# Optimization experiments

Hardware: AMD Instinct MI355X
Metric: run time of the kernel (lower is better)

The kernel has to match this reference:

```python
import jax, jax.numpy as jnp
import numpy as np

N = 50000       # nodes
E = 800000      # directed edges (src -> dst)
INDIM, HID, OUT = 256, 128, 64
NEG_SLOPE = 0.2  # PyG GATConv default negative_slope


def gat_layer(x, src, dst, W, a_src, a_dst, b, n_nodes):
    """Single-head PyG-style GATConv with self-loops already in (src, dst)."""
    h = x @ W.T                                   # [N, F_out]
    alpha_src = h @ a_src                         # [N]
    alpha_dst = h @ a_dst                         # [N]
    # per-edge attention logits, LeakyReLU
    e = jax.nn.leaky_relu(alpha_src[src] + alpha_dst[dst], NEG_SLOPE)  # [E']
    # segment softmax grouped by destination node (numerically stable)
    m = jnp.full((n_nodes,), -jnp.inf, e.dtype).at[dst].max(e)
    ee = jnp.exp(e - m[dst])
    denom = jax.ops.segment_sum(ee, dst, num_segments=n_nodes)
    alpha = ee / denom[dst]                       # [E']
    # weighted scatter-add of source messages
    out = jax.ops.segment_sum(h[src] * alpha[:, None], dst, num_segments=n_nodes)
    return out + b


def setup_inputs() -> dict:
    key = jax.random.key(0)
    ks = jax.random.split(key, 10)
    s = 0.1
    return {
        "x": jax.random.normal(ks[0], (N, INDIM), jnp.float32),
        "edge_index": jax.random.randint(ks[1], (2, E), 0, N, dtype=jnp.int32),
        "W1": jax.random.normal(ks[2], (HID, INDIM), jnp.float32) * s,
        "a_src1": jax.random.normal(ks[3], (HID,), jnp.float32) * s,
        "a_dst1": jax.random.normal(ks[4], (HID,), jnp.float32) * s,
        "b1": jnp.zeros((HID,), jnp.float32),
        "W2": jax.random.normal(ks[5], (OUT, HID), jnp.float32) * s,
        "a_src2": jax.random.normal(ks[6], (OUT,), jnp.float32) * s,
        "a_dst2": jax.random.normal(ks[7], (OUT,), jnp.float32) * s,
        "b2": jnp.zeros((OUT,), jnp.float32),
    }


def reference(x, edge_index, W1, a_src1, a_dst1, b1, W2, a_src2, a_dst2, b2):
    n_nodes = x.shape[0]
    # PyG GATConv default add_self_loops=True
    loops = jnp.arange(n_nodes, dtype=edge_index.dtype)
    src = jnp.concatenate([edge_index[0], loops])
    dst = jnp.concatenate([edge_index[1], loops])
    h = gat_layer(x, src, dst, W1, a_src1, a_dst1, b1, n_nodes)
    h = jax.nn.relu(h)
    h = gat_layer(h, src, dst, W2, a_src2, a_dst2, b2, n_nodes)
    return h
```

## Files before the change

### kernel.cpp

```cpp
#include <hip/hip_runtime.h>
#include <hip/hip_bf16.h>
#include <math.h>

#define NN 50000
#define EE 800000
#define INDIM 256
#define HID 128
#define OUTF 64
#define NEG_SLOPE 0.2f
#define CAP 64

#define NB ((NN + 255) >> 8)
#define BCAP 6144
#define CHUNK 2048
#define EPT 8
#define BPAD 16

typedef __attribute__((ext_vector_type(8))) short bf16x8;
typedef __attribute__((ext_vector_type(4))) float f32x4;

__device__ inline float bflo(unsigned p) { return __uint_as_float(p << 16); }
__device__ inline float bfhi(unsigned p) { return __uint_as_float(p & 0xffff0000u); }
__device__ inline unsigned f2bf(float f) {
    unsigned u = __float_as_uint(f);
    return (u + 0x7fffu + ((u >> 16) & 1u)) >> 16;
}
__device__ inline unsigned cvt_pk_bf16(float lo, float hi) {
    unsigned r;
    asm("v_cvt_pk_bf16_f32 %0, %1, %2" : "=v"(r) : "v"(lo), "v"(hi));
    return r;
}
__device__ inline float leaky(float l) { return (l > 0.f) ? l : NEG_SLOPE * l; }

template <typename AT, int BM, int BN, int WR, int WC, bool FA, bool FAL>
__device__ inline void gemm_body(const AT* __restrict__ A,
                                 const float* __restrict__ B,
                                 unsigned short* __restrict__ Cb,
                                 const float* __restrict__ a_s,
                                 const float* __restrict__ a_d,
                                 float* __restrict__ asrc,
                                 float* __restrict__ adst,
                                 int N, int K, int bid)
{
    constexpr int LD = 40;
    constexpr int MF = (BM / WR) / 16;
    constexpr int NF = (BN / WC) / 16;
    constexpr int NA  = (sizeof(AT) == 4) ? (BM * 8 / 256) : (BM * 4 / 256);
    constexpr int NBL = BN * 8 / 256;
    static_assert(!FA || WC == 1, "register alpha needs full cols per wave");
    __shared__ unsigned short As[BM * LD];
    __shared__ unsigned short Bs[BN * LD];
    __shared__ float al_s[FAL ? 2 * BM : 2];

    const int tid = threadIdx.x;
    const int wave = tid >> 6, lane = tid & 63;
    const int wr = wave / WC, wc = wave % WC;
    const int wrow0 = wr * (BM / WR);
    const int wcol0 = wc * (BN / WC);
    const int row0 = bid * BM;
    const int lrow = lane & 15, lkg = lane >> 4;

    if constexpr (FAL) {
        for (int i = tid; i < 2 * BM; i += 256) al_s[i] = 0.f;
    }

    int arow[NA], aoff[NA]; bool aval[NA];
    #pragma unroll
    for (int u = 0; u < NA; ++u) {
        int i = u * 256 + tid;
        if constexpr (sizeof(AT) == 4) { arow[u] = i >> 3; aoff[u] = (i & 7) * 4; }
        else                           { arow[u] = i >> 2; aoff[u] = (i & 3) * 8; }
        aval[u] = (row0 + arow[u]) < N;
    }
    int brow[NBL], boff[NBL];
    #pragma unroll
    for (int u = 0; u < NBL; ++u) {
        int i = u * 256 + tid;
        brow[u] = i >> 3; boff[u] = (i & 7) * 4;
    }

    uint4 ra[NA], rb[NBL];
    auto loadA = [&](int k0) {
        #pragma unroll
        for (int u = 0; u < NA; ++u) {
            ra[u] = make_uint4(0u, 0u, 0u, 0u);
            if (aval[u])
                ra[u] = *(const uint4*)((const AT*)A + (size_t)(row0 + arow[u]) * K + k0 + aoff[u]);
        }
    };
    auto loadB = [&](int k0) {
        #pragma unroll
        for (int u = 0; u < NBL; ++u)
            rb[u] = *(const uint4*)(B + (size_t)brow[u] * K + k0 + boff[u]);
    };
    auto storeLDS = [&]() {
        if constexpr (sizeof(AT) == 4) {
            #pragma unroll
            for (int u = 0; u < NA; ++u) {
                unsigned p0 = cvt_pk_bf16(__uint_as_float(ra[u].x), __uint_as_float(ra[u].y));
                unsigned p1 = cvt_pk_bf16(__uint_as_float(ra[u].z), __uint_as_float(ra[u].w));
                *(uint2*)&As[arow[u] * LD + aoff[u]] = make_uint2(p0, p1);
            }
        } else {
            #pragma unroll
            for (int u = 0; u < NA; ++u)
                *(uint4*)&As[arow[u] * LD + aoff[u]] = ra[u];
        }
        #pragma unroll
        for (int u = 0; u < NBL; ++u) {
            unsigned p0 = cvt_pk_bf16(__uint_as_float(rb[u].x), __uint_as_float(rb[u].y));
            unsigned p1 = cvt_pk_bf16(__uint_as_float(rb[u].z), __uint_as_float(rb[u].w));
            *(uint2*)&Bs[brow[u] * LD + boff[u]] = make_uint2(p0, p1);
        }
    };

    f32x4 acc[MF][NF];
    #pragma unroll
    for (int mi = 0; mi < MF; ++mi)
        #pragma unroll
        for (int ni = 0; ni < NF; ++ni) acc[mi][ni] = 0.f;

    const int NK = K / 32;
    loadA(0); loadB(0);
    for (int ks = 0; ks < NK; ++ks) {
        storeLDS();
        __syncthreads();
        if (ks + 1 < NK) { loadA((ks + 1) * 32); loadB((ks + 1) * 32); }

        bf16x8 af[MF], bfr[NF];
        #pragma unroll
        for (int mi = 0; mi < MF; ++mi)
            af[mi] = *(const bf16x8*)&As[(wrow0 + mi * 16 + lrow) * LD + lkg * 8];
        #pragma unroll
        for (int ni = 0; ni < NF; ++ni)
            bfr[ni] = *(const bf16x8*)&Bs[(wcol0 + ni * 16 + lrow) * LD + lkg * 8];
        #pragma unroll
        for (int mi = 0; mi < MF; ++mi)
            #pragma unroll
            for (int ni = 0; ni < NF; ++ni)
                acc[mi][ni] = __builtin_amdgcn_mfma_f32_16x16x32_bf16(
                    af[mi], bfr[ni], acc[mi][ni], 0, 0, 0);
        __syncthreads();
    }

    if constexpr (FA || FAL) {
        float asv[NF], adv[NF];
        #pragma unroll
        for (int ni = 0; ni < NF; ++ni) {
            int c = wcol0 + ni * 16 + lrow;
            asv[ni] = a_s[c]; adv[ni] = a_d[c];
        }
        #pragma unroll
        for (int mi = 0; mi < MF; ++mi)
            #pragma unroll
            for (int r = 0; r < 4; ++r) {
                float ps = 0.f, pd = 0.f;
                #pragma unroll
                for (int ni = 0; ni < NF; ++ni) {
                    ps = fmaf(acc[mi][ni][r], asv[ni], ps);
                    pd = fmaf(acc[mi][ni][r], adv[ni], pd);
                }
                #pragma unroll
                for (int d = 1; d < 16; d <<= 1) {
                    ps += __shfl_xor(ps, d);
                    pd += __shfl_xor(pd, d);
                }
                int lr_ = wrow0 + mi * 16 + lkg * 4 + r;
                if constexpr (FA) {
                    int gr = row0 + lr_;
                    if (lrow == 0 && gr < N) { asrc[gr] = ps; adst[gr] = pd; }
                } else {
                    if (lrow == 0) {
                        atomicAdd(&al_s[lr_], ps);
                        atomicAdd(&al_s[BM + lr_], pd);
                    }
                }
            }
    }

    #pragma unroll
    for (int mi = 0; mi < MF; ++mi)
        #pragma unroll
        for (int ni = 0; ni < NF; ++ni)
            #pragma unroll
            for (int r = 0; r < 4; ++r) {
                int gr = row0 + wrow0 + mi * 16 + lkg * 4 + r;
                int gc = wcol0 + ni * 16 + lrow;
                if (gr < N)
                    Cb[(size_t)gr * BN + gc] = (unsigned short)f2bf(acc[mi][ni][r]);
            }

    if constexpr (FAL) {
        __syncthreads();
        if (tid < BM) {
            int gr = row0 + tid;
            if (gr < N) { asrc[gr] = al_s[tid]; adst[gr] = al_s[BM + tid]; }
        }
    }
}

__global__ __launch_bounds__(256) void gemm1_kernel(
    const float* __restrict__ x, const float* __restrict__ W1,
    unsigned short* __restrict__ h1b,
    const float* __restrict__ a_s, const float* __restrict__ a_d,
    float* __restrict__ asrc, float* __restrict__ adst, int N, int K)
{
    gemm_body<float, 64, 128, 2, 2, false, true>(x, W1, h1b, a_s, a_d,
                                                 asrc, adst, N, K, blockIdx.x);
}

__global__ __launch_bounds__(256) void gemm2_alpha_kernel(
    const unsigned short* __restrict__ A, const float* __restrict__ B,
    unsigned short* __restrict__ Cb,
    const float* __restrict__ a_s, const float* __restrict__ a_d,
    float* __restrict__ asrc, float* __restrict__ adst, int N, int K)
{
    gemm_body<unsigned short, 64, 64, 4, 1, true, false>(A, B, Cb, a_s, a_d,
                                                         asrc, adst, N, K, blockIdx.x);
}

__global__ __launch_bounds__(256) void bin_kernel(
    const int* __restrict__ src_in, const int* __restrict__ dst_in,
    unsigned* __restrict__ gbucket, int* __restrict__ bcnt,
    int E, int tot)
{
    __shared__ int h_hist[256];
    __shared__ int h_scan[256];
    __shared__ int h_ofs[256];
    __shared__ int h_gbase[256];
    __shared__ unsigned grp[CHUNK];

    const int tid = threadIdx.x;
    const int e0 = blockIdx.x * CHUNK;
    const int cntc = min(CHUNK, tot - e0);

    h_hist[tid] = 0;
    __syncthreads();

    unsigned pk[EPT];
    bool val[EPT];
    #pragma unroll
    for (int u = 0; u < EPT; ++u) {
        int e = e0 + u * 256 + tid;
        val[u] = (e < tot);
        if (val[u]) {
            int d, s;
            if (e < E) { d = dst_in[e]; s = src_in[e]; }
            else       { d = e - E;    s = d; }
            pk[u] = ((unsigned)d << 16) | (unsigned)s;
            atomicAdd(&h_hist[d >> 8], 1);
        }
    }
    __syncthreads();

    int v = h_hist[tid];
    int incl = v;
    h_scan[tid] = incl;
    __syncthreads();
    for (int off = 1; off < 256; off <<= 1) {
        int t = (tid >= off) ? h_scan[tid - off] : 0;
        __syncthreads();
        incl += t;
        h_scan[tid] = incl;
        __syncthreads();
    }
    int excl = incl - v;
    h_scan[tid] = excl;
    h_ofs[tid] = excl;
    h_gbase[tid] = (tid < NB && v > 0) ? atomicAdd(&bcnt[tid * BPAD], v) : 0;
    __syncthreads();

    #pragma unroll
    for (int u = 0; u < EPT; ++u)
        if (val[u]) {
            int b = pk[u] >> 24;
            int pos = atomicAdd(&h_ofs[b], 1);
            grp[pos] = pk[u];
        }
    __syncthreads();

    for (int i = tid; i < cntc; i += 256) {
        unsigned p = grp[i];
        int b = p >> 24;
        int gp = h_gbase[b] + (i - h_scan[b]);
        if (gp < BCAP) gbucket[(size_t)b * BCAP + gp] = p;
    }
}

__global__ __launch_bounds__(256) void csr_build(
    const unsigned* __restrict__ gbucket, const int* __restrict__ bcnt,
    int* __restrict__ cnt, unsigned short* __restrict__ csr, int N)
{
    __shared__ int c2[256];
    __shared__ unsigned short cl[256 * CAP];

    const int b = blockIdx.x;
    const int tid = threadIdx.x;
    c2[tid] = 0;
    __syncthreads();

    int len = bcnt[b * BPAD];
    if (len > BCAP) len = BCAP;
    for (int i = tid; i < len; i += 256) {
        unsigned p = gbucket[(size_t)b * BCAP + i];
        int dl = (p >> 16) & 255;
        int s  = p & 0xffff;
        int r = atomicAdd(&c2[dl], 1);
        if (r < CAP) cl[(dl << 6) + r] = (unsigned short)s;
    }
    __syncthreads();

    int d = (b << 8) + tid;
    if (d < N) cnt[d] = c2[tid];

    int rows = N - (b << 8);
    rows = (rows > 256) ? 256 : rows;
    const uint4* sp = (const uint4*)cl;
    uint4* dp = (uint4*)(csr + (((size_t)b << 8) << 6));
    for (int i = tid; i < rows * 8; i += 256) dp[i] = sp[i];
}

template <int F, bool RELU, bool OUTBF>
__global__ __launch_bounds__(256) void aggregate_kernel(
    const unsigned short* __restrict__ hb, const unsigned short* __restrict__ csr,
    const int* __restrict__ cnt_arr, const float* __restrict__ asrc,
    const float* __restrict__ adst, const float* __restrict__ bias,
    void* __restrict__ outv, int n)
{
    constexpr int G = F / 8;
    constexpr int EPI = 64 / G;
    constexpr int STEP = EPI * 4;
    int wave = (int)((blockIdx.x * (size_t)blockDim.x + threadIdx.x) >> 6);
    int lane = threadIdx.x & 63;
    if (wave >= n) return;
    const size_t beg = (size_t)wave << 6;
    int cntv = cnt_arr[wave];
    cntv = (cntv > CAP) ? CAP : cntv;
    const float ad = adst[wave];
    const int grp = lane / G, fl = lane % G;

    float acc[8];
    #pragma unroll
    for (int p = 0; p < 8; ++p) acc[p] = 0.f;

    int s = 0;
    float e = 0.f;
    if (lane < cntv) { s = (int)csr[beg + lane]; e = __expf(leaky(asrc[s] + ad)); }
    float denom = e;
    #pragma unroll
    for (int d = 32; d > 0; d >>= 1) denom += __shfl_xor(denom, d);
    float w = e * __fdividef(1.f, denom);

    for (int jj0 = 0; jj0 < cntv; jj0 += STEP) {
        uint4 q[4];
        float wj[4];
        #pragma unroll
        for (int u = 0; u < 4; ++u) {
            int sel = jj0 + u * EPI + grp;
            int sj = __shfl(s, sel);
            wj[u] = __shfl(w, sel);
            q[u] = make_uint4(0u, 0u, 0u, 0u);
            if (sel < cntv)
                q[u] = *(const uint4*)(hb + (size_t)sj * F + fl * 8);
        }
        #pragma unroll
        for (int u = 0; u < 4; ++u) {
            acc[0] += wj[u] * bflo(q[u].x); acc[1] += wj[u] * bfhi(q[u].x);
            acc[2] += wj[u] * bflo(q[u].y); acc[3] += wj[u] * bfhi(q[u].y);
            acc[4] += wj[u] * bflo(q[u].z); acc[5] += wj[u] * bfhi(q[u].z);
            acc[6] += wj[u] * bflo(q[u].w); acc[7] += wj[u] * bfhi(q[u].w);
        }
    }

    #pragma unroll
    for (int d = G; d < 64; d <<= 1)
        #pragma unroll
        for (int p = 0; p < 8; ++p) acc[p] += __shfl_xor(acc[p], d);

    if (lane < G) {
        float v[8];
        #pragma unroll
        for (int p = 0; p < 8; ++p) {
            v[p] = acc[p] + bias[fl * 8 + p];
            if (RELU) v[p] = fmaxf(v[p], 0.f);
        }
        if constexpr (OUTBF) {
            unsigned short* o = (unsigned short*)outv + (size_t)wave * F + fl * 8;
            uint4 pk;
            pk.x = cvt_pk_bf16(v[0], v[1]);
            pk.y = cvt_pk_bf16(v[2], v[3]);
            pk.z = cvt_pk_bf16(v[4], v[5]);
            pk.w = cvt_pk_bf16(v[6], v[7]);
            *(uint4*)o = pk;
        } else {
            float* o = (float*)outv + (size_t)wave * F + fl * 8;
            *(float4*)o       = make_float4(v[0], v[1], v[2], v[3]);
            *(float4*)(o + 4) = make_float4(v[4], v[5], v[6], v[7]);
        }
    }
}

extern "C" void kernel_launch(void* const* d_in, const int* in_sizes, int n_in,
                              void* d_out, int out_size, void* d_ws, size_t ws_size,
                              hipStream_t stream)
{
    const float* x      = (const float*)d_in[0];
    const int*   ei     = (const int*)d_in[1];
    const float* W1     = (const float*)d_in[2];
    const float* a_src1 = (const float*)d_in[3];
    const float* a_dst1 = (const float*)d_in[4];
    const float* b1     = (const float*)d_in[5];
    const float* W2     = (const float*)d_in[6];
    const float* a_src2 = (const float*)d_in[7];
    const float* a_dst2 = (const float*)d_in[8];
    const float* b2     = (const float*)d_in[9];
    float* out = (float*)d_out;

    const int N = NN, E = EE;
    const int* src_in = ei;
    const int* dst_in = ei + E;

    char* p = (char*)d_ws;
    unsigned short* h1b   = (unsigned short*)p; p += (size_t)N * HID * 2;
    unsigned short* hmidb = (unsigned short*)p; p += (size_t)N * HID * 2;
    unsigned short* h2b   = (unsigned short*)p; p += (size_t)N * OUTF * 2;
    float* asrc = (float*)p; p += (size_t)N * 4;
    float* adst = (float*)p; p += (size_t)N * 4;
    int* cnt    = (int*)p;   p += (size_t)N * 4;
    unsigned short* csr = (unsigned short*)p; p += (size_t)N * CAP * 2;
    int* bcnt = (int*)p; p += (size_t)NB * BPAD * 4;
    unsigned* gbucket = (unsigned*)h2b;

    hipMemsetAsync(bcnt, 0, (size_t)NB * BPAD * 4, stream);

    const int GB   = (N + 63) / 64;
    const int BINB = (E + N + CHUNK - 1) / CHUNK;
    const int nwb  = (N * 64 + 255) / 256;

    bin_kernel<<<BINB, 256, 0, stream>>>(src_in, dst_in, gbucket, bcnt, E, E + N);
    csr_build<<<NB, 256, 0, stream>>>(gbucket, bcnt, cnt, csr, N);

    gemm1_kernel<<<GB, 256, 0, stream>>>(x, W1, h1b, a_src1, a_dst1,
                                         asrc, adst, N, INDIM);
    aggregate_kernel<HID, true, true><<<nwb, 256, 0, stream>>>(
        h1b, csr, cnt, asrc, adst, b1, hmidb, N);

    gemm2_alpha_kernel<<<GB, 256, 0, stream>>>(hmidb, W2, h2b, a_src2, a_dst2,
                                               asrc, adst, N, HID);
    aggregate_kernel<OUTF, false, false><<<nwb, 256, 0, stream>>>(
        h2b, csr, cnt, asrc, adst, b2, out, N);

    (void)in_sizes; (void)n_in; (void)out_size; (void)ws_size;
}
```

Baseline: 206.2 us.

## Fuse gemm1 with edge binning and layer-1 aggregation with gemm2

The layer-1 GEMM and the edge binning kernel now run as one launch, with block-index ranges dispatching to either body so the two independent jobs share the GPU. The layer-1 aggregation is fused with the layer-2 GEMM: each 256-thread block aggregates 64 nodes into a bf16 tile in shared memory, then runs MFMA against W2 and computes the layer-2 attention scalars. This removes the hidden-feature round trip through global memory and two launches. In exchange, the aggregation runs with far fewer blocks, each wave handling 16 nodes in sequence, which may reduce latency hiding for the gathers.

```diff
diff --git a/kernel.cpp b/kernel.cpp
--- a/kernel.cpp
+++ b/kernel.cpp
@@ -32,7 +32,7 @@
 }
 __device__ inline float leaky(float l) { return (l > 0.f) ? l : NEG_SLOPE * l; }
 
-template <typename AT, int BM, int BN, int WR, int WC, bool FA, bool FAL>
+template <typename AT, int BM, int BN, int WR, int WC, bool FAL>
 __device__ inline void gemm_body(const AT* __restrict__ A,
                                  const float* __restrict__ B,
                                  unsigned short* __restrict__ Cb,
@@ -47,7 +47,6 @@
     constexpr int NF = (BN / WC) / 16;
     constexpr int NA  = (sizeof(AT) == 4) ? (BM * 8 / 256) : (BM * 4 / 256);
     constexpr int NBL = BN * 8 / 256;
-    static_assert(!FA || WC == 1, "register alpha needs full cols per wave");
     __shared__ unsigned short As[BM * LD];
     __shared__ unsigned short Bs[BN * LD];
     __shared__ float al_s[FAL ? 2 * BM : 2];
@@ -143,7 +142,7 @@
         __syncthreads();
     }
 
-    if constexpr (FA || FAL) {
+    if constexpr (FAL) {
         float asv[NF], adv[NF];
         #pragma unroll
         for (int ni = 0; ni < NF; ++ni) {
@@ -166,14 +165,9 @@
                     pd += __shfl_xor(pd, d);
                 }
                 int lr_ = wrow0 + mi * 16 + lkg * 4 + r;
-                if constexpr (FA) {
-                    int gr = row0 + lr_;
-                    if (lrow == 0 && gr < N) { asrc[gr] = ps; adst[gr] = pd; }
-                } else {
-                    if (lrow == 0) {
-                        atomicAdd(&al_s[lr_], ps);
-                        atomicAdd(&al_s[BM + lr_], pd);
-                    }
+                if (lrow == 0) {
+                    atomicAdd(&al_s[lr_], ps);
+                    atomicAdd(&al_s[BM + lr_], pd);
                 }
             }
     }
@@ -199,30 +193,12 @@
     }
 }
 
-__global__ __launch_bounds__(256) void gemm1_kernel(
-    const float* __restrict__ x, const float* __restrict__ W1,
-    unsigned short* __restrict__ h1b,
-    const float* __restrict__ a_s, const float* __restrict__ a_d,
-    float* __restrict__ asrc, float* __restrict__ adst, int N, int K)
-{
-    gemm_body<float, 64, 128, 2, 2, false, true>(x, W1, h1b, a_s, a_d,
-                                                 asrc, adst, N, K, blockIdx.x);
-}
-
-__global__ __launch_bounds__(256) void gemm2_alpha_kernel(
-    const unsigned short* __restrict__ A, const float* __restrict__ B,
-    unsigned short* __restrict__ Cb,
-    const float* __restrict__ a_s, const float* __restrict__ a_d,
-    float* __restrict__ asrc, float* __restrict__ adst, int N, int K)
-{
-    gemm_body<unsigned short, 64, 64, 4, 1, true, false>(A, B, Cb, a_s, a_d,
-                                                         asrc, adst, N, K, blockIdx.x);
-}
-
-__global__ __launch_bounds__(256) void bin_kernel(
-    const int* __restrict__ src_in, const int* __restrict__ dst_in,
-    unsigned* __restrict__ gbucket, int* __restrict__ bcnt,
-    int E, int tot)
+__device__ inline void bin_body(int bb,
+                                const int* __restrict__ src_in,
+                                const int* __restrict__ dst_in,
+                                unsigned* __restrict__ gbucket,
+                                int* __restrict__ bcnt,
+                                int E, int tot)
 {
     __shared__ int h_hist[256];
     __shared__ int h_scan[256];
@@ -231,7 +207,7 @@
     __shared__ unsigned grp[CHUNK];
 
     const int tid = threadIdx.x;
-    const int e0 = blockIdx.x * CHUNK;
+    const int e0 = bb * CHUNK;
     const int cntc = min(CHUNK, tot - e0);
 
     h_hist[tid] = 0;
@@ -287,6 +263,23 @@
     }
 }
 
+__global__ __launch_bounds__(256) void fused_gemm1_bin(
+    const float* __restrict__ x, const float* __restrict__ W1,
+    unsigned short* __restrict__ h1b,
+    const float* __restrict__ a_s, const float* __restrict__ a_d,
+    float* __restrict__ asrc, float* __restrict__ adst,
+    const int* __restrict__ src_in, const int* __restrict__ dst_in,
+    unsigned* __restrict__ gbucket, int* __restrict__ bcnt,
+    int N, int K, int GB, int E)
+{
+    if ((int)blockIdx.x < GB) {
+        gemm_body<float, 64, 128, 2, 2, true>(x, W1, h1b, a_s, a_d,
+                                              asrc, adst, N, K, blockIdx.x);
+    } else {
+        bin_body(blockIdx.x - GB, src_in, dst_in, gbucket, bcnt, E, E + N);
+    }
+}
+
 __global__ __launch_bounds__(256) void csr_build(
     const unsigned* __restrict__ gbucket, const int* __restrict__ bcnt,
     int* __restrict__ cnt, unsigned short* __restrict__ csr, int N)
@@ -318,6 +311,146 @@
     const uint4* sp = (const uint4*)cl;
     uint4* dp = (uint4*)(csr + (((size_t)b << 8) << 6));
     for (int i = tid; i < rows * 8; i += 256) dp[i] = sp[i];
+}
+
+__global__ __launch_bounds__(256) void agg1_gemm2_kernel(
+    const unsigned short* __restrict__ h1b, const unsigned short* __restrict__ csr,
+    const int* __restrict__ cnt_arr, const float* __restrict__ asrc1,
+    const float* __restrict__ adst1, const float* __restrict__ b1,
+    const float* __restrict__ W2, const float* __restrict__ a_s2,
+    const float* __restrict__ a_d2, unsigned short* __restrict__ h2b,
+    float* __restrict__ asrc2, float* __restrict__ adst2, int N)
+{
+    constexpr int F = HID, G = 16, EPI = 4, STEP = 16;
+    constexpr int LDH = 136;
+    __shared__ unsigned short hm[64 * LDH];
+    __shared__ unsigned short Bs[64 * 40];
+
+    const int tid = threadIdx.x;
+    const int wv = tid >> 6, lane = tid & 63;
+    const int base = (int)blockIdx.x * 64;
+    const int grp = lane / G, fl = lane % G;
+
+    float bs[8];
+    *(float4*)&bs[0] = *(const float4*)(b1 + fl * 8);
+    *(float4*)&bs[4] = *(const float4*)(b1 + fl * 8 + 4);
+
+    for (int i = 0; i < 16; ++i) {
+        const int row = i * 4 + wv;
+        const int node = base + row;
+        float acc[8];
+        #pragma unroll
+        for (int p = 0; p < 8; ++p) acc[p] = 0.f;
+
+        if (node < N) {
+            const size_t beg = (size_t)node << 6;
+            int cntv = cnt_arr[node];
+            cntv = (cntv > CAP) ? CAP : cntv;
+            const float ad = adst1[node];
+
+            int s = 0;
+            float e = 0.f;
+            if (lane < cntv) { s = (int)csr[beg + lane]; e = __expf(leaky(asrc1[s] + ad)); }
+            float denom = e;
+            #pragma unroll
+            for (int d = 32; d > 0; d >>= 1) denom += __shfl_xor(denom, d);
+            float w = e * __fdividef(1.f, denom);
+
+            for (int jj0 = 0; jj0 < cntv; jj0 += STEP) {
+                uint4 q[4];
+                float wj[4];
+                #pragma unroll
+                for (int u = 0; u < 4; ++u) {
+                    int sel = jj0 + u * EPI + grp;
+                    int sj = __shfl(s, sel);
+                    wj[u] = __shfl(w, sel);
+                    q[u] = make_uint4(0u, 0u, 0u, 0u);
+                    if (sel < cntv)
+                        q[u] = *(const uint4*)(h1b + (size_t)sj * F + fl * 8);
+                }
+                #pragma unroll
+                for (int u = 0; u < 4; ++u) {
+                    acc[0] += wj[u] * bflo(q[u].x); acc[1] += wj[u] * bfhi(q[u].x);
+                    acc[2] += wj[u] * bflo(q[u].y); acc[3] += wj[u] * bfhi(q[u].y);
+                    acc[4] += wj[u] * bflo(q[u].z); acc[5] += wj[u] * bfhi(q[u].z);
+                    acc[6] += wj[u] * bflo(q[u].w); acc[7] += wj[u] * bfhi(q[u].w);
+                }
+            }
+            #pragma unroll
+            for (int d = G; d < 64; d <<= 1)
+                #pragma unroll
+                for (int p = 0; p < 8; ++p) acc[p] += __shfl_xor(acc[p], d);
+
+            #pragma unroll
+            for (int p = 0; p < 8; ++p) acc[p] = fmaxf(acc[p] + bs[p], 0.f);
+        }
+        if (lane < G) {
+            uint4 pk;
+            pk.x = cvt_pk_bf16(acc[0], acc[1]);
+            pk.y = cvt_pk_bf16(acc[2], acc[3]);
+            pk.z = cvt_pk_bf16(acc[4], acc[5]);
+            pk.w = cvt_pk_bf16(acc[6], acc[7]);
+            *(uint4*)&hm[row * LDH + lane * 8] = pk;
+        }
+    }
+    __syncthreads();
+
+    const int lrow = lane & 15, lkg = lane >> 4;
+    f32x4 acc2[4];
+    #pragma unroll
+    for (int ni = 0; ni < 4; ++ni) acc2[ni] = 0.f;
+
+    for (int k0 = 0; k0 < HID; k0 += 32) {
+        #pragma unroll
+        for (int it = tid; it < 64 * 8; it += 256) {
+            int rw = it >> 3, kq = it & 7;
+            float4 v = *(const float4*)(W2 + (size_t)rw * HID + k0 + kq * 4);
+            unsigned p0 = cvt_pk_bf16(v.x, v.y);
+            unsigned p1 = cvt_pk_bf16(v.z, v.w);
+            *(uint2*)&Bs[rw * 40 + kq * 4] = make_uint2(p0, p1);
+        }
+        __syncthreads();
+        bf16x8 af = *(const bf16x8*)&hm[(wv * 16 + lrow) * LDH + k0 + lkg * 8];
+        #pragma unroll
+        for (int ni = 0; ni < 4; ++ni) {
+            bf16x8 bfr = *(const bf16x8*)&Bs[(ni * 16 + lrow) * 40 + lkg * 8];
+            acc2[ni] = __builtin_amdgcn_mfma_f32_16x16x32_bf16(af, bfr, acc2[ni], 0, 0, 0);
+        }
+        __syncthreads();
+    }
+
+    float asv[4], adv[4];
+    #pragma unroll
+    for (int ni = 0; ni < 4; ++ni) {
+        int c = ni * 16 + lrow;
+        asv[ni] = a_s2[c]; adv[ni] = a_d2[c];
+    }
+    #pragma unroll
+    for (int r = 0; r < 4; ++r) {
+        float ps = 0.f, pd = 0.f;
+        #pragma unroll
+        for (int ni = 0; ni < 4; ++ni) {
+            ps = fmaf(acc2[ni][r], asv[ni], ps);
+            pd = fmaf(acc2[ni][r], adv[ni], pd);
+        }
+        #pragma unroll
+        for (int d = 1; d < 16; d <<= 1) {
+            ps += __shfl_xor(ps, d);
+            pd += __shfl_xor(pd, d);
+        }
+        int gr = base + wv * 16 + lkg * 4 + r;
+        if (lrow == 0 && gr < N) { asrc2[gr] = ps; adst2[gr] = pd; }
+    }
+
+    #pragma unroll
+    for (int ni = 0; ni < 4; ++ni)
+        #pragma unroll
+        for (int r = 0; r < 4; ++r) {
+            int gr = base + wv * 16 + lkg * 4 + r;
+            int gc = ni * 16 + lrow;
+            if (gr < N)
+                h2b[(size_t)gr * OUTF + gc] = (unsigned short)f2bf(acc2[ni][r]);
+        }
 }
 
 template <int F, bool RELU, bool OUTBF>
@@ -422,10 +555,11 @@
 
     char* p = (char*)d_ws;
     unsigned short* h1b   = (unsigned short*)p; p += (size_t)N * HID * 2;
-    unsigned short* hmidb = (unsigned short*)p; p += (size_t)N * HID * 2;
     unsigned short* h2b   = (unsigned short*)p; p += (size_t)N * OUTF * 2;
-    float* asrc = (float*)p; p += (size_t)N * 4;
-    float* adst = (float*)p; p += (size_t)N * 4;
+    float* asrc  = (float*)p; p += (size_t)N * 4;
+    float* adst  = (float*)p; p += (size_t)N * 4;
+    float* asrc2 = (float*)p; p += (size_t)N * 4;
+    float* adst2 = (float*)p; p += (size_t)N * 4;
     int* cnt    = (int*)p;   p += (size_t)N * 4;
     unsigned short* csr = (unsigned short*)p; p += (size_t)N * CAP * 2;
     int* bcnt = (int*)p; p += (size_t)NB * BPAD * 4;
@@ -437,18 +571,17 @@
     const int BINB = (E + N + CHUNK - 1) / CHUNK;
     const int nwb  = (N * 64 + 255) / 256;
 
-    bin_kernel<<<BINB, 256, 0, stream>>>(src_in, dst_in, gbucket, bcnt, E, E + N);
+    fused_gemm1_bin<<<GB + BINB, 256, 0, stream>>>(
+        x, W1, h1b, a_src1, a_dst1, asrc, adst, src_in, dst_in,
+        gbucket, bcnt, N, INDIM, GB, E);
     csr_build<<<NB, 256, 0, stream>>>(gbucket, bcnt, cnt, csr, N);
 
-    gemm1_kernel<<<GB, 256, 0, stream>>>(x, W1, h1b, a_src1, a_dst1,
-                                         asrc, adst, N, INDIM);
-    aggregate_kernel<HID, true, true><<<nwb, 256, 0, stream>>>(
-        h1b, csr, cnt, asrc, adst, b1, hmidb, N);
-
-    gemm2_alpha_kernel<<<GB, 256, 0, stream>>>(hmidb, W2, h2b, a_src2, a_dst2,
-                                               asrc, adst, N, HID);
+    agg1_gemm2_kernel<<<GB, 256, 0, stream>>>(
+        h1b, csr, cnt, asrc, adst, b1, W2, a_src2, a_dst2,
+        h2b, asrc2, adst2, N);
+
     aggregate_kernel<OUTF, false, false><<<nwb, 256, 0, stream>>>(
-        h2b, csr, cnt, asrc, adst, b2, out, N);
+        h2b, csr, cnt, asrc2, adst2, b2, out, N);
 
     (void)in_sizes; (void)n_in; (void)out_size; (void)ws_size;
 }
```

Result: no change. 203.7 us (-1.2%).
